# Optimization experiments

Hardware: AMD Instinct MI355X
Metric: run time of the kernel (lower is better)

The kernel has to match this reference:

```python
import jax, jax.numpy as jnp
import numpy as np

BN_EPS = 1e-5


def conv1d(x, w, pad):
    # x: [N, Cin, L], w: [Cout, Cin, K] -> [N, Cout, L]
    return jax.lax.conv_general_dilated(
        x, w, window_strides=(1,), padding=[(pad, pad)],
        dimension_numbers=("NCH", "OIH", "NCH"))


def setup_inputs() -> dict:
    key = jax.random.key(0)
    k1, k2, k3, k4 = jax.random.split(key, 4)
    b, c, h, w = 32, 512, 64, 64
    x = jax.random.normal(k1, (b, c, h, w), jnp.float32)
    # ECA-style channel conv: kernel_size=5 for channel=512
    w1 = jax.random.normal(k2, (1, 1, 5), jnp.float32) * 0.3
    # Spatial convs created in forward: Conv1d(h,h,3) and Conv1d(w,w,3)
    wh = jax.random.normal(k3, (h, h, 3), jnp.float32) * (1.0 / np.sqrt(3.0 * h))
    ww = jax.random.normal(k4, (w, w, 3), jnp.float32) * (1.0 / np.sqrt(3.0 * w))
    gamma = jnp.ones((1,), jnp.float32)
    beta = jnp.zeros((1,), jnp.float32)
    return {"x": x, "w1": w1, "wh": wh, "ww": ww, "gamma": gamma, "beta": beta}


def reference(x, w1, wh, ww, gamma, beta):
    b, c, h, w = x.shape
    # Channel attention: global avg pool -> conv1d over channel axis -> sigmoid
    f1 = jnp.mean(x, axis=(2, 3)).reshape(b, 1, c)          # [b,1,c]
    f1 = conv1d(f1, w1, pad=2).reshape(b, c, 1, 1)
    f1 = jax.nn.sigmoid(f1)
    F = x * f1
    # Spatial attention: channel-mean -> conv1d along w (channels=h) + conv1d along h (channels=w)
    f2 = jnp.mean(x, axis=1)                                 # [b,h,w]
    f2_h = conv1d(f2, wh, pad=1).reshape(b, 1, h, w)
    f2_w = conv1d(jnp.transpose(f2, (0, 2, 1)), ww, pad=1)   # [b,w,h]
    f2_w = jnp.transpose(f2_w, (0, 2, 1)).reshape(b, 1, h, w)
    f2 = f2_h + f2_w
    # BatchNorm2d(1), training-mode batch statistics over (b, h, w)
    mu = jnp.mean(f2)
    var = jnp.mean(jnp.square(f2 - mu))
    f2 = gamma[0] * (f2 - mu) * jax.lax.rsqrt(var + BN_EPS) + beta[0]
    return F * jax.nn.sigmoid(f2)
```

## Files before the change

### kernel.cpp

```cpp
#include <hip/hip_runtime.h>

#define NB 32
#define NC 512
#define NH 64
#define NW 64
#define NHW 4096
#define NTOT ((size_t)NB * NC * NHW)

typedef float f32x4 __attribute__((ext_vector_type(4)));

#define OFF_S1PART 0
#define OFF_F2PART 65536
#define OFF_F1SIG  1114112
#define OFF_F2RAW  1130496
#define OFF_BNPART 1261568

__global__ __launch_bounds__(256) void k_reduce(const float* __restrict__ x,
                                                float* __restrict__ s1part,
                                                float* __restrict__ f2part) {
  __shared__ float lds_s1[64][4];
  const int bid = blockIdx.x;
  const int jc = bid & 3;
  const int cg = (bid >> 2) & 7;
  const int b = bid >> 5;
  const int tid = threadIdx.x;
  const int lane = tid & 63;
  const int wv = tid >> 6;
  const int j0 = jc * 1024 + tid * 4;
  const float* xb = x + ((size_t)(b * NC + cg * 64)) * NHW + j0;
  float a0 = 0.f, a1 = 0.f, a2 = 0.f, a3 = 0.f;
  for (int c = 0; c < 64; ++c) {
    const f32x4 v = *reinterpret_cast<const f32x4*>(xb + (size_t)c * NHW);
    a0 += v.x; a1 += v.y; a2 += v.z; a3 += v.w;
    float s = (v.x + v.y) + (v.z + v.w);
#pragma unroll
    for (int off = 32; off > 0; off >>= 1) s += __shfl_down(s, off);
    if (lane == 0) lds_s1[c][wv] = s;
  }
  __syncthreads();
  if (tid < 64) {
    const float s =
        lds_s1[tid][0] + lds_s1[tid][1] + lds_s1[tid][2] + lds_s1[tid][3];
    s1part[(b * NC + cg * 64 + tid) * 4 + jc] = s;
  }
  f32x4 o;
  o.x = a0; o.y = a1; o.z = a2; o.w = a3;
  *reinterpret_cast<f32x4*>(f2part + ((size_t)cg * NB + b) * NHW + j0) = o;
}

__global__ __launch_bounds__(256) void k_f2(const float* __restrict__ f2part,
                                            const float* __restrict__ s1part,
                                            const float* __restrict__ w1,
                                            const float* __restrict__ wh,
                                            const float* __restrict__ ww,
                                            float* __restrict__ f2raw,
                                            float* __restrict__ bnpart,
                                            float* __restrict__ f1sig) {
  __shared__ float mp[66][66];
  __shared__ float wwT[192][66];
  __shared__ float red[8];
  const int b = blockIdx.x >> 4;
  const int rg = blockIdx.x & 15;
  const int tid = threadIdx.x;

  if (tid < 66) {
    mp[0][tid] = 0.f;
    mp[65][tid] = 0.f;
    mp[tid][0] = 0.f;
    mp[tid][65] = 0.f;
  }
  for (int t = tid; t < 64 * 192; t += 256) wwT[t % 192][t / 192] = ww[t];
  for (int t = tid; t < NHW; t += 256) {
    float s = 0.f;
#pragma unroll
    for (int cg = 0; cg < 8; ++cg)
      s += f2part[((size_t)(cg * NB + b)) * NHW + t];
    mp[1 + (t >> 6)][1 + (t & 63)] = s * (1.0f / (float)NC);
  }
  __syncthreads();

  const int i = rg * 4 + (tid >> 6);
  const int j = tid & 63;
  const float* whp = wh + 192 * __builtin_amdgcn_readfirstlane(i);
  float acc = 0.f;
#pragma unroll 16
  for (int ic = 0; ic < 64; ++ic) {
    acc += whp[ic * 3 + 0] * mp[ic + 1][j] +
           whp[ic * 3 + 1] * mp[ic + 1][j + 1] +
           whp[ic * 3 + 2] * mp[ic + 1][j + 2];
    acc += wwT[ic * 3 + 0][j] * mp[i][ic + 1] +
           wwT[ic * 3 + 1][j] * mp[i + 1][ic + 1] +
           wwT[ic * 3 + 2][j] * mp[i + 2][ic + 1];
  }
  f2raw[(size_t)b * NHW + (i << 6) + j] = acc;

  float lsum = acc, lsq = acc * acc;
#pragma unroll
  for (int off = 32; off > 0; off >>= 1) {
    lsum += __shfl_down(lsum, off);
    lsq += __shfl_down(lsq, off);
  }
  if ((tid & 63) == 0) {
    red[(tid >> 6) * 2 + 0] = lsum;
    red[(tid >> 6) * 2 + 1] = lsq;
  }
  __syncthreads();
  if (tid == 0) {
    bnpart[blockIdx.x * 2 + 0] = red[0] + red[2] + red[4] + red[6];
    bnpart[blockIdx.x * 2 + 1] = red[1] + red[3] + red[5] + red[7];
  }

  if (rg == 0) {
#pragma unroll
    for (int c0 = 0; c0 < 512; c0 += 256) {
      const int c = c0 + tid;
      float acc5 = 0.f;
#pragma unroll
      for (int k = 0; k < 5; ++k) {
        const int cc = c + k - 2;
        if (cc >= 0 && cc < NC) {
          const f32x4 sp = reinterpret_cast<const f32x4*>(s1part)[b * NC + cc];
          acc5 += w1[k] * ((sp.x + sp.y) + (sp.z + sp.w));
        }
      }
      acc5 *= (1.0f / (float)NHW);
      f1sig[b * NC + c] = 1.0f / (1.0f + __expf(-acc5));
    }
  }
}

__global__ __launch_bounds__(256) void k_out(const float* __restrict__ x,
                                             const float* __restrict__ f1sig,
                                             const float* __restrict__ f2raw,
                                             const float* __restrict__ bnpart,
                                             const float* __restrict__ gamma,
                                             const float* __restrict__ beta,
                                             float* __restrict__ out) {
  __shared__ float bnv[2];
  const int tid = threadIdx.x;
  if (tid < 64) {
    float s = 0.f, q = 0.f;
#pragma unroll
    for (int r = 0; r < 8; ++r) {
      s += bnpart[2 * (tid + 64 * r) + 0];
      q += bnpart[2 * (tid + 64 * r) + 1];
    }
#pragma unroll
    for (int off = 32; off > 0; off >>= 1) {
      s += __shfl_down(s, off);
      q += __shfl_down(q, off);
    }
    if (tid == 0) {
      const float N = (float)(NB * NHW);
      const float mu = s / N;
      const float var = q / N - mu * mu;
      bnv[0] = mu;
      bnv[1] = gamma[0] * rsqrtf(var + 1e-5f);
    }
  }
  __syncthreads();
  const float mu = bnv[0];
  const float g = bnv[1];
  const float bt = beta[0];

  const size_t total4 = NTOT / 4;
  const size_t stride = (size_t)gridDim.x * blockDim.x;
  for (size_t v = (size_t)blockIdx.x * blockDim.x + tid; v < total4;
       v += stride) {
    const int hw4 = (int)(v & 1023);
    const int bc = (int)(v >> 10);
    const int b = bc >> 9;
    const float f1 = f1sig[bc];
    const f32x4 xv = reinterpret_cast<const f32x4*>(x)[v];
    const f32x4 fv =
        reinterpret_cast<const f32x4*>(f2raw)[(size_t)(b << 10) + hw4];
    f32x4 ov;
    ov.x = xv.x * f1 * (1.0f / (1.0f + __expf(-(g * (fv.x - mu) + bt))));
    ov.y = xv.y * f1 * (1.0f / (1.0f + __expf(-(g * (fv.y - mu) + bt))));
    ov.z = xv.z * f1 * (1.0f / (1.0f + __expf(-(g * (fv.z - mu) + bt))));
    ov.w = xv.w * f1 * (1.0f / (1.0f + __expf(-(g * (fv.w - mu) + bt))));
    __builtin_nontemporal_store(ov, reinterpret_cast<f32x4*>(out) + v);
  }
}

extern "C" void kernel_launch(void* const* d_in, const int* in_sizes, int n_in,
                              void* d_out, int out_size, void* d_ws,
                              size_t ws_size, hipStream_t stream) {
  const float* x = (const float*)d_in[0];
  const float* w1 = (const float*)d_in[1];
  const float* wh = (const float*)d_in[2];
  const float* ww = (const float*)d_in[3];
  const float* gamma = (const float*)d_in[4];
  const float* beta = (const float*)d_in[5];
  float* out = (float*)d_out;
  float* ws = (float*)d_ws;

  float* s1part = ws + OFF_S1PART;
  float* f2part = ws + OFF_F2PART;
  float* f1sig = ws + OFF_F1SIG;
  float* f2raw = ws + OFF_F2RAW;
  float* bnpart = ws + OFF_BNPART;

  k_reduce<<<NB * 8 * 4, 256, 0, stream>>>(x, s1part, f2part);
  k_f2<<<NB * 16, 256, 0, stream>>>(f2part, s1part, w1, wh, ww, f2raw, bnpart,
                                    f1sig);
  k_out<<<2048, 256, 0, stream>>>(x, f1sig, f2raw, bnpart, gamma, beta, out);
}
```

Measured before the change: 165.1 us.

## Restructure channel reduction per wave and batch-loop the output kernel

The reduce kernel now gives each wave 16 channels, with four independent vector loads in flight per channel. It collects per-channel sums through xor shuffles kept in registers instead of an LDS write per channel, then combines the per-wave spatial partials in LDS with a single barrier. The output kernel replaces the grid-stride loop with a fixed mapping where each thread covers one spatial/channel slot across all 32 batches. It uses nontemporal loads for x. This aims to raise memory-level parallelism and cut per-iteration index math and LDS traffic, in exchange for larger LDS usage and a hardcoded grid assumption of 2048 blocks.

```diff
diff --git a/kernel.cpp b/kernel.cpp
--- a/kernel.cpp
+++ b/kernel.cpp
@@ -18,7 +18,7 @@
 __global__ __launch_bounds__(256) void k_reduce(const float* __restrict__ x,
                                                 float* __restrict__ s1part,
                                                 float* __restrict__ f2part) {
-  __shared__ float lds_s1[64][4];
+  __shared__ f32x4 comb[4][256];
   const int bid = blockIdx.x;
   const int jc = bid & 3;
   const int cg = (bid >> 2) & 7;
@@ -26,26 +26,37 @@
   const int tid = threadIdx.x;
   const int lane = tid & 63;
   const int wv = tid >> 6;
-  const int j0 = jc * 1024 + tid * 4;
-  const float* xb = x + ((size_t)(b * NC + cg * 64)) * NHW + j0;
-  float a0 = 0.f, a1 = 0.f, a2 = 0.f, a3 = 0.f;
-  for (int c = 0; c < 64; ++c) {
-    const f32x4 v = *reinterpret_cast<const f32x4*>(xb + (size_t)c * NHW);
-    a0 += v.x; a1 += v.y; a2 += v.z; a3 += v.w;
-    float s = (v.x + v.y) + (v.z + v.w);
-#pragma unroll
-    for (int off = 32; off > 0; off >>= 1) s += __shfl_down(s, off);
-    if (lane == 0) lds_s1[c][wv] = s;
-  }
-  __syncthreads();
-  if (tid < 64) {
-    const float s =
-        lds_s1[tid][0] + lds_s1[tid][1] + lds_s1[tid][2] + lds_s1[tid][3];
-    s1part[(b * NC + cg * 64 + tid) * 4 + jc] = s;
-  }
-  f32x4 o;
-  o.x = a0; o.y = a1; o.z = a2; o.w = a3;
-  *reinterpret_cast<f32x4*>(f2part + ((size_t)cg * NB + b) * NHW + j0) = o;
+
+  const size_t base =
+      ((size_t)(b * NC + cg * 64 + wv * 16)) * NHW + jc * 1024 + lane * 4;
+  f32x4 p0 = {0.f, 0.f, 0.f, 0.f}, p1 = p0, p2 = p0, p3 = p0;
+  float myS = 0.f;
+#pragma unroll
+  for (int k = 0; k < 16; ++k) {
+    const float* xc = x + base + (size_t)k * NHW;
+    const f32x4 v0 = *reinterpret_cast<const f32x4*>(xc + 0);
+    const f32x4 v1 = *reinterpret_cast<const f32x4*>(xc + 256);
+    const f32x4 v2 = *reinterpret_cast<const f32x4*>(xc + 512);
+    const f32x4 v3 = *reinterpret_cast<const f32x4*>(xc + 768);
+    p0 += v0; p1 += v1; p2 += v2; p3 += v3;
+    const f32x4 t = (v0 + v1) + (v2 + v3);
+    float s = (t.x + t.y) + (t.z + t.w);
+#pragma unroll
+    for (int m = 32; m > 0; m >>= 1) s += __shfl_xor(s, m);
+    myS = (lane == k) ? s : myS;
+  }
+  if (lane < 16)
+    s1part[(b * NC + cg * 64 + wv * 16 + lane) * 4 + jc] = myS;
+
+  comb[wv][0 * 64 + lane] = p0;
+  comb[wv][1 * 64 + lane] = p1;
+  comb[wv][2 * 64 + lane] = p2;
+  comb[wv][3 * 64 + lane] = p3;
+  __syncthreads();
+  const f32x4 r =
+      (comb[0][tid] + comb[1][tid]) + (comb[2][tid] + comb[3][tid]);
+  reinterpret_cast<f32x4*>(f2part)[((size_t)cg * NB + b) * 1024 + jc * 256 +
+                                   tid] = r;
 }
 
 __global__ __launch_bounds__(256) void k_f2(const float* __restrict__ f2part,
@@ -163,23 +174,24 @@
   const float g = bnv[1];
   const float bt = beta[0];
 
-  const size_t total4 = NTOT / 4;
-  const size_t stride = (size_t)gridDim.x * blockDim.x;
-  for (size_t v = (size_t)blockIdx.x * blockDim.x + tid; v < total4;
-       v += stride) {
-    const int hw4 = (int)(v & 1023);
-    const int bc = (int)(v >> 10);
-    const int b = bc >> 9;
-    const float f1 = f1sig[bc];
-    const f32x4 xv = reinterpret_cast<const f32x4*>(x)[v];
-    const f32x4 fv =
-        reinterpret_cast<const f32x4*>(f2raw)[(size_t)(b << 10) + hw4];
+  const int gid = blockIdx.x * 256 + tid;
+  const int hw4 = gid & 1023;
+  const int cq = gid >> 10;
+  const f32x4* xp = reinterpret_cast<const f32x4*>(x) + gid;
+  const f32x4* fp = reinterpret_cast<const f32x4*>(f2raw) + hw4;
+  const float* f1p = f1sig + cq;
+  f32x4* op = reinterpret_cast<f32x4*>(out) + gid;
+
+  for (int b = 0; b < NB; ++b) {
+    const f32x4 xv = __builtin_nontemporal_load(xp + (size_t)b * 524288);
+    const f32x4 fv = fp[(size_t)b * 1024];
+    const float f1 = f1p[(size_t)b * 512];
     f32x4 ov;
     ov.x = xv.x * f1 * (1.0f / (1.0f + __expf(-(g * (fv.x - mu) + bt))));
     ov.y = xv.y * f1 * (1.0f / (1.0f + __expf(-(g * (fv.y - mu) + bt))));
     ov.z = xv.z * f1 * (1.0f / (1.0f + __expf(-(g * (fv.z - mu) + bt))));
     ov.w = xv.w * f1 * (1.0f / (1.0f + __expf(-(g * (fv.w - mu) + bt))));
-    __builtin_nontemporal_store(ov, reinterpret_cast<f32x4*>(out) + v);
+    __builtin_nontemporal_store(ov, op + (size_t)b * 524288);
   }
 }
 
```

Result: slower. 170.0 us (+3.0%).
